# Optimization experiments

Hardware: AMD Instinct MI355X
Metric: run time of the kernel (lower is better)

Reference implementation:

```python
import jax, jax.numpy as jnp
import numpy as np

SCORE_THRESHOLD = 0.5
IOU_THRESHOLD = 0.5


def _pairwise_iou(boxes):
    # boxes: [N, 4] in xyxy
    x1, y1, x2, y2 = boxes[:, 0], boxes[:, 1], boxes[:, 2], boxes[:, 3]
    area = (x2 - x1) * (y2 - y1)  # [N]
    ix1 = jnp.maximum(x1[:, None], x1[None, :])
    iy1 = jnp.maximum(y1[:, None], y1[None, :])
    ix2 = jnp.minimum(x2[:, None], x2[None, :])
    iy2 = jnp.minimum(y2[:, None], y2[None, :])
    iw = jnp.clip(ix2 - ix1, 0.0)
    ih = jnp.clip(iy2 - iy1, 0.0)
    inter = iw * ih  # [N, N]
    union = area[:, None] + area[None, :] - inter
    return inter / jnp.maximum(union, 1e-9)


def setup_inputs() -> dict:
    key = jax.random.key(0)
    rtdetr_raw_out = jax.random.uniform(key, (1, 8192, 5), dtype=jnp.float32)
    return {"rtdetr_raw_out": rtdetr_raw_out}


def reference(rtdetr_raw_out):
    x = rtdetr_raw_out[0]                      # [N, 5]
    cxcywh = x[:, :4]
    conf = x[:, 4]
    conf = conf / jnp.max(conf)                # normalize by max score
    cx, cy, w, h = cxcywh[:, 0], cxcywh[:, 1], cxcywh[:, 2], cxcywh[:, 3]
    xyxy = jnp.stack([cx - w * 0.5, cy - h * 0.5, cx + w * 0.5, cy + h * 0.5], axis=1)
    valid = conf >= SCORE_THRESHOLD            # score filter
    N = xyxy.shape[0]
    # sort by descending score (torchvision nms processes boxes in score order)
    order = jnp.argsort(-conf)
    boxes_s = xyxy[order]
    scores_s = conf[order]
    valid_s = valid[order]
    iou = _pairwise_iou(boxes_s)               # [N, N]
    idx = jnp.arange(N)

    def body(i, keep):
        # if box i survives, suppress all lower-score boxes with IoU > thr
        sup = keep[i] & (iou[i] > IOU_THRESHOLD) & (idx > i)
        return keep & ~sup

    keep = jax.lax.fori_loop(0, N, body, valid_s)
    out = jnp.concatenate([boxes_s, scores_s[:, None]], axis=1)  # [N, 5]
    # fixed-shape output: suppressed / below-threshold rows are zeroed
    return jnp.where(keep[:, None], out, 0.0)
```

## Files before the change

### kernel.cpp

```cpp
#include <hip/hip_runtime.h>
#include <cstdint>

typedef unsigned long long ull;

#define N_BOX 8192
#define N_WORDS 128
#define CH 512
#define WPC 8

#define OFF_TB     0
#define OFF_TC     3440640
#define OFF_TD     3932160
#define OFF_BOXES  4456448
#define OFF_SCORES 4587520
#define OFF_RANK   4620288
#define OFF_MAXC   4653056

__device__ __forceinline__ int rows_before2(int c) {
    return 7424 * c - 256 * c * c;
}

__device__ __forceinline__ ull make_key(float s, int idx) {
    return (((ull)__float_as_uint(s)) << 13) | (ull)(8191 - idx);
}

__device__ __forceinline__ float box_area(float4 b) {
    return __fmul_rn(__fsub_rn(b.z, b.x), __fsub_rn(b.w, b.y));
}

__device__ __forceinline__ bool iou_gt_half(float4 a, float aarea, float4 b, float barea) {
    float ix1 = fmaxf(a.x, b.x);
    float iy1 = fmaxf(a.y, b.y);
    float ix2 = fminf(a.z, b.z);
    float iy2 = fminf(a.w, b.w);
    float iw = fmaxf(__fsub_rn(ix2, ix1), 0.0f);
    float ih = fmaxf(__fsub_rn(iy2, iy1), 0.0f);
    float inter = __fmul_rn(iw, ih);
    float uni = __fsub_rn(__fadd_rn(aarea, barea), inter);
    float iou = __fdiv_rn(inter, fmaxf(uni, 1e-9f));
    return iou > 0.5f;
}

__global__ __launch_bounds__(256) void k1_max_zero(const float* __restrict__ in,
                                                   int* __restrict__ maxci,
                                                   int* __restrict__ rank) {
    int t = threadIdx.x;
    int i = blockIdx.x * 256 + t;
    float c = in[i * 5 + 4];
    for (int off = 32; off; off >>= 1) c = fmaxf(c, __shfl_down(c, off));
    __shared__ float wm[4];
    if ((t & 63) == 0) wm[t >> 6] = c;
    __syncthreads();
    if (t == 0) {
        float m = fmaxf(fmaxf(wm[0], wm[1]), fmaxf(wm[2], wm[3]));
        atomicMax(maxci, __float_as_int(m));
    }
    rank[i] = 0;
}

__global__ __launch_bounds__(256) void k2_rank(const float* __restrict__ in,
                                               const float* __restrict__ maxc_p,
                                               int* __restrict__ rank) {
    __shared__ ull keys[1024];
    int t = threadIdx.x;
    int bx = blockIdx.x;
    int it = bx & 31;
    int jt = bx >> 5;
    float maxc = *maxc_p;
    for (int r = 0; r < 4; ++r) {
        int j = jt * 1024 + r * 256 + t;
        float s = __fdiv_rn(in[j * 5 + 4], maxc);
        keys[r * 256 + t] = make_key(s, j);
    }
    __syncthreads();
    int i = it * 256 + t;
    ull ki = make_key(__fdiv_rn(in[i * 5 + 4], maxc), i);
    int cnt = 0;
    #pragma unroll 8
    for (int k = 0; k < 1024; ++k) cnt += (keys[k] > ki) ? 1 : 0;
    atomicAdd(&rank[i], cnt);
}

__global__ __launch_bounds__(256) void k3_scatter(const float* __restrict__ in,
                                                  const int* __restrict__ rank,
                                                  const float* __restrict__ maxc_p,
                                                  float4* __restrict__ boxes4,
                                                  float* __restrict__ scores) {
    int i = blockIdx.x * 256 + threadIdx.x;
    float cx = in[i * 5 + 0];
    float cy = in[i * 5 + 1];
    float w  = in[i * 5 + 2];
    float h  = in[i * 5 + 3];
    float c  = in[i * 5 + 4];
    float maxc = *maxc_p;
    float s = __fdiv_rn(c, maxc);
    int r = rank[i];
    float4 b;
    b.x = __fsub_rn(cx, __fmul_rn(w, 0.5f));
    b.y = __fsub_rn(cy, __fmul_rn(h, 0.5f));
    b.z = __fadd_rn(cx, __fmul_rn(w, 0.5f));
    b.w = __fadd_rn(cy, __fmul_rn(h, 0.5f));
    boxes4[r] = b;
    scores[r] = s;
}

__global__ __launch_bounds__(256) void k4_build(const float4* __restrict__ boxes4,
                                                const float* __restrict__ scores,
                                                ull* __restrict__ TB,
                                                ull* __restrict__ TC,
                                                ull* __restrict__ TD) {
    __shared__ float4 sb[CH];
    __shared__ float sa[CH];
    int bid = blockIdx.x;
    int t = threadIdx.x;
    int c;
    int mode;
    int j0;
    if (bid >= 1920) {
        mode = 2;
        int d = bid - 1920;
        c = d >> 4;
        j0 = (d & 15) * 32;
    } else if (bid >= 1680) {
        mode = 1;
        int d = bid - 1680;
        c = d >> 4;
        j0 = (d & 15) * 32;
    } else {
        mode = 0;
        c = 0;
        int rem = bid;
        while (rem >= 224 - 16 * c) { rem -= 224 - 16 * c; ++c; }
        j0 = CH * (c + 2) + rem * 32;
    }
    if (scores[c * CH] < 0.5f) return;
    if (mode == 0 && scores[j0] < 0.5f) return;

    for (int i = t; i < CH; i += 256) {
        float4 b = boxes4[c * CH + i];
        sb[i] = b;
        sa[i] = box_area(b);
    }
    __syncthreads();

    int w = t & 7;
    int r = t >> 3;
    if (mode == 2) {
        int jl = j0 + r;
        float4 me = sb[jl];
        float ma = sa[jl];
        int wj = jl >> 6;
        int lim = (w < wj) ? 64 : ((w == wj) ? (jl & 63) : 0);
        ull bits = 0;
        for (int k = 0; k < lim; ++k)
            if (iou_gt_half(sb[w * 64 + k], sa[w * 64 + k], me, ma)) bits |= 1ull << k;
        TD[c * 4096 + w * 512 + jl] = bits;
    } else if (mode == 1) {
        int jl = j0 + r;
        int j = CH * (c + 1) + jl;
        float4 me = boxes4[j];
        float ma = box_area(me);
        ull bits = 0;
        for (int k = 0; k < 64; ++k)
            if (iou_gt_half(sb[w * 64 + k], sa[w * 64 + k], me, ma)) bits |= 1ull << k;
        TC[c * 4096 + w * 512 + jl] = bits;
    } else {
        int j = j0 + r;
        float4 me = boxes4[j];
        float ma = box_area(me);
        ull bits = 0;
        for (int k = 0; k < 64; ++k)
            if (iou_gt_half(sb[w * 64 + k], sa[w * 64 + k], me, ma)) bits |= 1ull << k;
        TB[(size_t)(rows_before2(c) + (j - CH * (c + 2))) * WPC + w] = bits;
    }
}

__global__ __launch_bounds__(1024) void k5_nms(const float4* __restrict__ boxes4,
                                               const float* __restrict__ scores,
                                               const ull* __restrict__ TBg,
                                               const ull* __restrict__ TCg,
                                               const ull* __restrict__ TDg,
                                               float* __restrict__ out) {
    __shared__ ull TDb[2][CH * WPC];
    __shared__ ull TCb[2][CH * WPC];
    __shared__ unsigned amask32[2 * N_WORDS];
    __shared__ ull keptbuf[2][WPC];
    __shared__ int svb;
    int t = threadIdx.x;
    int lane = t & 63;
    int wave = t >> 6;

    if (t == 0) svb = 0;
    __syncthreads();
    {
        int cnt = 0;
        #pragma unroll
        for (int k = 0; k < 8; ++k) cnt += (scores[k * 1024 + t] >= 0.5f) ? 1 : 0;
        for (int off = 32; off; off >>= 1) cnt += __shfl_down(cnt, off);
        if (lane == 0) atomicAdd(&svb, cnt);
    }
    {
        const ulonglong2* src = (const ulonglong2*)TDg;
        ulonglong2* dst = (ulonglong2*)TDb[0];
        #pragma unroll
        for (int i2 = t; i2 < CH * WPC / 2; i2 += 1024) dst[i2] = src[i2];
    }
    if (t < WPC) { keptbuf[0][t] = 0; keptbuf[1][t] = 0; }
    __syncthreads();
    int vb = svb;

    if (t < 2 * N_WORDS) {
        int n = vb - t * 32;
        amask32[t] = (n >= 32) ? 0xffffffffu : ((n <= 0) ? 0u : ((1u << n) - 1u));
    }
    __syncthreads();

    int nchv = (vb + CH - 1) / CH;
    for (int c = 0; c < nchv; ++c) {
        int cur = c & 1;
        if (wave == 0) {
            ull alive[WPC];
            #pragma unroll
            for (int w = 0; w < WPC; ++w)
                alive[w] = (ull)amask32[c * 16 + 2 * w] |
                           ((ull)amask32[c * 16 + 2 * w + 1] << 32);
            if (c > 0) {
                const ull* kb = keptbuf[(c - 1) & 1];
                const ull* TCc = TCb[cur];
                #pragma unroll
                for (int w = 0; w < WPC; ++w) {
                    ull kw = kb[w];
                    if (!kw) continue;
                    ull Tc2[WPC];
                    #pragma unroll
                    for (int v = 0; v < WPC; ++v)
                        Tc2[v] = TCc[w * 512 + v * 64 + lane];
                    #pragma unroll
                    for (int v = 0; v < WPC; ++v)
                        alive[v] &= ~__ballot((Tc2[v] & kw) != 0);
                }
            }
            const ull* T = TDb[cur];
            #pragma unroll
            for (int w = 0; w < WPC; ++w) {
                ull word = alive[w];
                if (!word) continue;
                ull Tc[WPC];
                #pragma unroll
                for (int j = 0; j < WPC; ++j)
                    if (j >= w) Tc[j] = T[w * 512 + j * 64 + lane];
                ull td = Tc[w];
                ull a2 = word, kept = 0;
                while (a2 & ~kept) {
                    bool al = (a2 >> lane) & 1;
                    bool kp = (kept >> lane) & 1;
                    ull nk = __ballot(al && !kp && ((td & a2) == 0));
                    ull nd = __ballot(al && !kp && ((td & kept) != 0));
                    kept |= nk;
                    a2 &= ~nd;
                }
                alive[w] = kept;
                #pragma unroll
                for (int j = 0; j < WPC; ++j) {
                    if (j <= w) continue;
                    if (!alive[j]) continue;
                    alive[j] &= ~__ballot((Tc[j] & kept) != 0);
                }
            }
            if (lane == 0) {
                #pragma unroll
                for (int w = 0; w < WPC; ++w) {
                    amask32[c * 16 + 2 * w]     = (unsigned)alive[w];
                    amask32[c * 16 + 2 * w + 1] = (unsigned)(alive[w] >> 32);
                    keptbuf[c & 1][w] = alive[w];
                }
            }
        } else if (wave < 8) {
            if (c > 0 && c - 1 <= 13) {
                const ull* kb = keptbuf[(c - 1) & 1];
                ull kw[WPC];
                ull anyk = 0;
                #pragma unroll
                for (int k = 0; k < WPC; ++k) { kw[k] = kb[k]; anyk |= kw[k]; }
                if (anyk) {
                    const ull* TBc = TBg + (size_t)rows_before2(c - 1) * WPC;
                    int jbase = CH * (c + 1);
                    int base = jbase + (t - 64);
                    unsigned am = 0;
                    int k = 0;
                    for (int j = base; j < vb; j += 448, ++k)
                        am |= (((amask32[j >> 5] >> (j & 31)) & 1u) << k);
                    while (am) {
                        int b1 = __builtin_ctz(am);
                        am &= am - 1;
                        bool had2 = (am != 0);
                        int b2 = had2 ? __builtin_ctz(am) : b1;
                        if (had2) am &= am - 1;
                        int j1 = base + b1 * 448;
                        int j2 = base + b2 * 448;
                        const ull* r1 = TBc + (size_t)(j1 - jbase) * WPC;
                        const ull* r2 = TBc + (size_t)(j2 - jbase) * WPC;
                        ull a1 = 0, a2v = 0;
                        #pragma unroll
                        for (int q = 0; q < WPC; ++q) a1 |= r1[q] & kw[q];
                        #pragma unroll
                        for (int q = 0; q < WPC; ++q) a2v |= r2[q] & kw[q];
                        if (a1) atomicAnd(&amask32[j1 >> 5], ~(1u << (j1 & 31)));
                        if (had2 && a2v) atomicAnd(&amask32[j2 >> 5], ~(1u << (j2 & 31)));
                    }
                }
            }
        } else {
            if (c + 1 < nchv) {
                const ulonglong2* tdsrc = (const ulonglong2*)(TDg + (c + 1) * CH * WPC);
                const ulonglong2* tcsrc = (const ulonglong2*)(TCg + c * CH * WPC);
                ulonglong2* tddst = (ulonglong2*)TDb[cur ^ 1];
                ulonglong2* tcdst = (ulonglong2*)TCb[cur ^ 1];
                #pragma unroll
                for (int i2 = t - 512; i2 < CH * WPC / 2; i2 += 512) {
                    tddst[i2] = tdsrc[i2];
                    tcdst[i2] = tcsrc[i2];
                }
            }
        }
        __syncthreads();
    }

    #pragma unroll
    for (int rr = 0; rr < 8; ++rr) {
        int j = t * 8 + rr;
        bool kept = (amask32[j >> 5] >> (j & 31)) & 1u;
        float4 b = boxes4[j];
        float s = scores[j];
        out[j * 5 + 0] = kept ? b.x : 0.0f;
        out[j * 5 + 1] = kept ? b.y : 0.0f;
        out[j * 5 + 2] = kept ? b.z : 0.0f;
        out[j * 5 + 3] = kept ? b.w : 0.0f;
        out[j * 5 + 4] = kept ? s   : 0.0f;
    }
}

extern "C" void kernel_launch(void* const* d_in, const int* in_sizes, int n_in,
                              void* d_out, int out_size, void* d_ws, size_t ws_size,
                              hipStream_t stream) {
    const float* in = (const float*)d_in[0];
    char* ws = (char*)d_ws;
    ull* TB        = (ull*)(ws + OFF_TB);
    ull* TC        = (ull*)(ws + OFF_TC);
    ull* TD        = (ull*)(ws + OFF_TD);
    float4* boxes4 = (float4*)(ws + OFF_BOXES);
    float* scores  = (float*)(ws + OFF_SCORES);
    int* rank      = (int*)(ws + OFF_RANK);
    float* maxc    = (float*)(ws + OFF_MAXC);
    float* out     = (float*)d_out;

    k1_max_zero<<<32, 256, 0, stream>>>(in, (int*)maxc, rank);
    k2_rank<<<256, 256, 0, stream>>>(in, maxc, rank);
    k3_scatter<<<32, 256, 0, stream>>>(in, rank, maxc, boxes4, scores);
    k4_build<<<2176, 256, 0, stream>>>(boxes4, scores, TB, TC, TD);
    k5_nms<<<1, 1024, 0, stream>>>(boxes4, scores, TB, TC, TD, out);
}
```

Baseline: 132.0 us.

## Split NMS across 16 blocks with cross-block flag handoff of kept masks

```diff
diff --git a/kernel.cpp b/kernel.cpp
--- a/kernel.cpp
+++ b/kernel.cpp
@@ -7,6 +7,7 @@
 #define N_WORDS 128
 #define CH 512
 #define WPC 8
+#define NBLK 16
 
 #define OFF_TB     0
 #define OFF_TC     3440640
@@ -15,6 +16,8 @@
 #define OFF_SCORES 4587520
 #define OFF_RANK   4620288
 #define OFF_MAXC   4653056
+#define OFF_CTRL   4653120
+#define OFF_KEPT   4653248
 
 __device__ __forceinline__ int rows_before2(int c) {
     return 7424 * c - 256 * c * c;
@@ -43,7 +46,8 @@
 
 __global__ __launch_bounds__(256) void k1_max_zero(const float* __restrict__ in,
                                                    int* __restrict__ maxci,
-                                                   int* __restrict__ rank) {
+                                                   int* __restrict__ rank,
+                                                   int* __restrict__ ctrl) {
     int t = threadIdx.x;
     int i = blockIdx.x * 256 + t;
     float c = in[i * 5 + 4];
@@ -55,6 +59,7 @@
         float m = fmaxf(fmaxf(wm[0], wm[1]), fmaxf(wm[2], wm[3]));
         atomicMax(maxci, __float_as_int(m));
     }
+    if (blockIdx.x == 0 && t < 32) ctrl[t] = 0;
     rank[i] = 0;
 }
 
@@ -85,7 +90,8 @@
                                                   const int* __restrict__ rank,
                                                   const float* __restrict__ maxc_p,
                                                   float4* __restrict__ boxes4,
-                                                  float* __restrict__ scores) {
+                                                  float* __restrict__ scores,
+                                                  int* __restrict__ ctrl) {
     int i = blockIdx.x * 256 + threadIdx.x;
     float cx = in[i * 5 + 0];
     float cy = in[i * 5 + 1];
@@ -102,6 +108,8 @@
     b.w = __fadd_rn(cy, __fmul_rn(h, 0.5f));
     boxes4[r] = b;
     scores[r] = s;
+    ull bal = __ballot(s >= 0.5f);
+    if ((threadIdx.x & 63) == 0) atomicAdd(&ctrl[16], (int)__popcll(bal));
 }
 
 __global__ __launch_bounds__(256) void k4_build(const float4* __restrict__ boxes4,
@@ -180,67 +188,92 @@
                                                const ull* __restrict__ TBg,
                                                const ull* __restrict__ TCg,
                                                const ull* __restrict__ TDg,
+                                               ull* __restrict__ keptg,
+                                               int* __restrict__ ctrl,
                                                float* __restrict__ out) {
-    __shared__ ull TDb[2][CH * WPC];
-    __shared__ ull TCb[2][CH * WPC];
-    __shared__ unsigned amask32[2 * N_WORDS];
-    __shared__ ull keptbuf[2][WPC];
-    __shared__ int svb;
+    __shared__ ull TDs[CH * WPC];
+    __shared__ ull TCs[CH * WPC];
+    __shared__ ull kwsh[WPC];
+    __shared__ unsigned amask[16];
+    int c = blockIdx.x;
     int t = threadIdx.x;
     int lane = t & 63;
     int wave = t >> 6;
-
-    if (t == 0) svb = 0;
-    __syncthreads();
-    {
-        int cnt = 0;
-        #pragma unroll
-        for (int k = 0; k < 8; ++k) cnt += (scores[k * 1024 + t] >= 0.5f) ? 1 : 0;
-        for (int off = 32; off; off >>= 1) cnt += __shfl_down(cnt, off);
-        if (lane == 0) atomicAdd(&svb, cnt);
-    }
-    {
-        const ulonglong2* src = (const ulonglong2*)TDg;
-        ulonglong2* dst = (ulonglong2*)TDb[0];
-        #pragma unroll
-        for (int i2 = t; i2 < CH * WPC / 2; i2 += 1024) dst[i2] = src[i2];
-    }
-    if (t < WPC) { keptbuf[0][t] = 0; keptbuf[1][t] = 0; }
-    __syncthreads();
-    int vb = svb;
-
-    if (t < 2 * N_WORDS) {
-        int n = vb - t * 32;
-        amask32[t] = (n >= 32) ? 0xffffffffu : ((n <= 0) ? 0u : ((1u << n) - 1u));
-    }
-    __syncthreads();
-
+    int vb = ctrl[16];
     int nchv = (vb + CH - 1) / CH;
-    for (int c = 0; c < nchv; ++c) {
-        int cur = c & 1;
+
+    if (c < nchv) {
+        {
+            const ulonglong2* src = (const ulonglong2*)(TDg + (size_t)c * CH * WPC);
+            ulonglong2* dst = (ulonglong2*)TDs;
+            #pragma unroll
+            for (int i2 = t; i2 < CH * WPC / 2; i2 += 1024) dst[i2] = src[i2];
+        }
+        if (c > 0) {
+            const ulonglong2* src = (const ulonglong2*)(TCg + (size_t)(c - 1) * CH * WPC);
+            ulonglong2* dst = (ulonglong2*)TCs;
+            #pragma unroll
+            for (int i2 = t; i2 < CH * WPC / 2; i2 += 1024) dst[i2] = src[i2];
+        }
+        if (t < 16) {
+            int n = vb - (c * 16 + t) * 32;
+            amask[t] = (n >= 32) ? 0xffffffffu : ((n <= 0) ? 0u : ((1u << n) - 1u));
+        }
+        __syncthreads();
+
+        for (int cp = 0; cp + 2 <= c; ++cp) {
+            if (wave == 0) {
+                if (lane == 0) { while (atomicAdd(&ctrl[cp], 0) == 0) {} }
+                __threadfence();
+                if (lane < WPC)
+                    kwsh[lane] = atomicAdd(&keptg[cp * WPC + lane], 0ull);
+            }
+            __syncthreads();
+            ull anyk = kwsh[0] | kwsh[1] | kwsh[2] | kwsh[3] |
+                       kwsh[4] | kwsh[5] | kwsh[6] | kwsh[7];
+            if (anyk && t < CH) {
+                if ((amask[t >> 5] >> (t & 31)) & 1u) {
+                    const ull* row = TBg +
+                        (size_t)(rows_before2(cp) + (c * CH + t - CH * (cp + 2))) * WPC;
+                    ull a = 0;
+                    #pragma unroll
+                    for (int q = 0; q < WPC; ++q) a |= row[q] & kwsh[q];
+                    if (a) atomicAnd(&amask[t >> 5], ~(1u << (t & 31)));
+                }
+            }
+            __syncthreads();
+        }
+
+        if (c > 0) {
+            if (wave == 0) {
+                if (lane == 0) { while (atomicAdd(&ctrl[c - 1], 0) == 0) {} }
+                __threadfence();
+                if (lane < WPC)
+                    kwsh[lane] = atomicAdd(&keptg[(c - 1) * WPC + lane], 0ull);
+            }
+            __syncthreads();
+            if (wave < WPC) {
+                bool dead = false;
+                #pragma unroll
+                for (int w = 0; w < WPC; ++w) {
+                    ull kw = kwsh[w];
+                    if (kw) dead |= (TCs[w * 512 + wave * 64 + lane] & kw) != 0ull;
+                }
+                ull d = __ballot(dead);
+                if (lane == 0 && d) {
+                    amask[2 * wave]     &= ~(unsigned)d;
+                    amask[2 * wave + 1] &= ~(unsigned)(d >> 32);
+                }
+            }
+            __syncthreads();
+        }
+
         if (wave == 0) {
             ull alive[WPC];
             #pragma unroll
             for (int w = 0; w < WPC; ++w)
-                alive[w] = (ull)amask32[c * 16 + 2 * w] |
-                           ((ull)amask32[c * 16 + 2 * w + 1] << 32);
-            if (c > 0) {
-                const ull* kb = keptbuf[(c - 1) & 1];
-                const ull* TCc = TCb[cur];
-                #pragma unroll
-                for (int w = 0; w < WPC; ++w) {
-                    ull kw = kb[w];
-                    if (!kw) continue;
-                    ull Tc2[WPC];
-                    #pragma unroll
-                    for (int v = 0; v < WPC; ++v)
-                        Tc2[v] = TCc[w * 512 + v * 64 + lane];
-                    #pragma unroll
-                    for (int v = 0; v < WPC; ++v)
-                        alive[v] &= ~__ballot((Tc2[v] & kw) != 0);
-                }
-            }
-            const ull* T = TDb[cur];
+                alive[w] = (ull)amask[2 * w] | ((ull)amask[2 * w + 1] << 32);
+            const ull* T = TDs;
             #pragma unroll
             for (int w = 0; w < WPC; ++w) {
                 ull word = alive[w];
@@ -270,66 +303,23 @@
             if (lane == 0) {
                 #pragma unroll
                 for (int w = 0; w < WPC; ++w) {
-                    amask32[c * 16 + 2 * w]     = (unsigned)alive[w];
-                    amask32[c * 16 + 2 * w + 1] = (unsigned)(alive[w] >> 32);
-                    keptbuf[c & 1][w] = alive[w];
-                }
-            }
-        } else if (wave < 8) {
-            if (c > 0 && c - 1 <= 13) {
-                const ull* kb = keptbuf[(c - 1) & 1];
-                ull kw[WPC];
-                ull anyk = 0;
-                #pragma unroll
-                for (int k = 0; k < WPC; ++k) { kw[k] = kb[k]; anyk |= kw[k]; }
-                if (anyk) {
-                    const ull* TBc = TBg + (size_t)rows_before2(c - 1) * WPC;
-                    int jbase = CH * (c + 1);
-                    int base = jbase + (t - 64);
-                    unsigned am = 0;
-                    int k = 0;
-                    for (int j = base; j < vb; j += 448, ++k)
-                        am |= (((amask32[j >> 5] >> (j & 31)) & 1u) << k);
-                    while (am) {
-                        int b1 = __builtin_ctz(am);
-                        am &= am - 1;
-                        bool had2 = (am != 0);
-                        int b2 = had2 ? __builtin_ctz(am) : b1;
-                        if (had2) am &= am - 1;
-                        int j1 = base + b1 * 448;
-                        int j2 = base + b2 * 448;
-                        const ull* r1 = TBc + (size_t)(j1 - jbase) * WPC;
-                        const ull* r2 = TBc + (size_t)(j2 - jbase) * WPC;
-                        ull a1 = 0, a2v = 0;
-                        #pragma unroll
-                        for (int q = 0; q < WPC; ++q) a1 |= r1[q] & kw[q];
-                        #pragma unroll
-                        for (int q = 0; q < WPC; ++q) a2v |= r2[q] & kw[q];
-                        if (a1) atomicAnd(&amask32[j1 >> 5], ~(1u << (j1 & 31)));
-                        if (had2 && a2v) atomicAnd(&amask32[j2 >> 5], ~(1u << (j2 & 31)));
-                    }
-                }
-            }
-        } else {
-            if (c + 1 < nchv) {
-                const ulonglong2* tdsrc = (const ulonglong2*)(TDg + (c + 1) * CH * WPC);
-                const ulonglong2* tcsrc = (const ulonglong2*)(TCg + c * CH * WPC);
-                ulonglong2* tddst = (ulonglong2*)TDb[cur ^ 1];
-                ulonglong2* tcdst = (ulonglong2*)TCb[cur ^ 1];
-                #pragma unroll
-                for (int i2 = t - 512; i2 < CH * WPC / 2; i2 += 512) {
-                    tddst[i2] = tdsrc[i2];
-                    tcdst[i2] = tcsrc[i2];
-                }
-            }
+                    atomicExch(&keptg[c * WPC + w], alive[w]);
+                    amask[2 * w]     = (unsigned)alive[w];
+                    amask[2 * w + 1] = (unsigned)(alive[w] >> 32);
+                }
+            }
+            __threadfence();
+            if (lane == 0) atomicExch(&ctrl[c], 1);
         }
         __syncthreads();
-    }
-
-    #pragma unroll
-    for (int rr = 0; rr < 8; ++rr) {
-        int j = t * 8 + rr;
-        bool kept = (amask32[j >> 5] >> (j & 31)) & 1u;
+    } else {
+        if (t < 16) amask[t] = 0u;
+        __syncthreads();
+    }
+
+    if (t < CH) {
+        int j = c * CH + t;
+        bool kept = (amask[t >> 5] >> (t & 31)) & 1u;
         float4 b = boxes4[j];
         float s = scores[j];
         out[j * 5 + 0] = kept ? b.x : 0.0f;
@@ -352,11 +342,13 @@
     float* scores  = (float*)(ws + OFF_SCORES);
     int* rank      = (int*)(ws + OFF_RANK);
     float* maxc    = (float*)(ws + OFF_MAXC);
+    int* ctrl      = (int*)(ws + OFF_CTRL);
+    ull* keptg     = (ull*)(ws + OFF_KEPT);
     float* out     = (float*)d_out;
 
-    k1_max_zero<<<32, 256, 0, stream>>>(in, (int*)maxc, rank);
+    k1_max_zero<<<32, 256, 0, stream>>>(in, (int*)maxc, rank, ctrl);
     k2_rank<<<256, 256, 0, stream>>>(in, maxc, rank);
-    k3_scatter<<<32, 256, 0, stream>>>(in, rank, maxc, boxes4, scores);
+    k3_scatter<<<32, 256, 0, stream>>>(in, rank, maxc, boxes4, scores, ctrl);
     k4_build<<<2176, 256, 0, stream>>>(boxes4, scores, TB, TC, TD);
-    k5_nms<<<1, 1024, 0, stream>>>(boxes4, scores, TB, TC, TD, out);
-}
+    k5_nms<<<NBLK, 1024, 0, stream>>>(boxes4, scores, TB, TC, TD, keptg, ctrl, out);
+}
```

Result: faster. 124.9 us (-5.3%).
